# Performance work log

Hardware: AMD Instinct MI355X
Metric: run time of the kernel (lower is better)

## Reference

```python
import jax, jax.numpy as jnp
import numpy as np

B = 16      # number of graphs (equal-sized, batch = repeat(arange(B), N))


def _knn_edges(pos, k, total):
    """Batch-aware kNN graph, torch_geometric knn_graph semantics.

    loop=False, flow='source_to_target': for each query node i, its k nearest
    neighbors j produce edges (row=j neighbor/source, col=i query/target).
    Returns (row, col) as flat global int32 index arrays of length B*N*k.
    """
    N = total // B
    posb = pos.reshape(B, N, -1)                      # [B, N, 3]
    sq = jnp.sum(posb * posb, axis=-1)                # [B, N]
    # squared Euclidean distances, [B, N, N]
    d2 = sq[:, :, None] + sq[:, None, :] - 2.0 * jnp.einsum('bnd,bmd->bnm', posb, posb)
    d2 = jnp.where(jnp.eye(N, dtype=bool)[None], jnp.inf, d2)  # exclude self-loops
    _, nbr = jax.lax.top_k(-d2, k)                    # [B, N, k] local neighbor idx
    offs = (jnp.arange(B, dtype=nbr.dtype) * N)[:, None, None]
    row = (nbr + offs).reshape(-1)                                      # neighbors (sources)
    col = jnp.broadcast_to(jnp.arange(N, dtype=nbr.dtype)[None, :, None] + offs,
                           (B, N, k)).reshape(-1)                       # query nodes (targets)
    return row, col


def reference(x, pos, batch, k):
    total = x.shape[0]
    row, col = _knn_edges(pos, k, total)
    # scatter_mean(x[col], row, dim_size=total): mean of gathered features per row index
    sums = jax.ops.segment_sum(x[col], row, num_segments=total)          # [total, d]
    cnt = jax.ops.segment_sum(jnp.ones(row.shape, x.dtype), row, num_segments=total)
    x_neigh_mean = sums / jnp.maximum(cnt, 1.0)[:, None]                 # empty rows -> 0
    return jnp.sum(jnp.abs(x - x_neigh_mean), axis=-1)                   # L1 norm, [total]


def setup_inputs() -> dict:
    key = jax.random.key(0)
    k1, k2 = jax.random.split(key)
    N = 4096
    x = jax.random.normal(k1, (B * N, 64), dtype=jnp.float32)
    pos = jax.random.normal(k2, (B * N, 3), dtype=jnp.float32)
    batch = jnp.repeat(jnp.arange(B, dtype=jnp.int64), N)
    return {"x": x, "pos": pos, "batch": batch, "k": 10}
```

## Files before the change

### kernel.cpp

```cpp
#include <hip/hip_runtime.h>
#include <stdint.h>

#define NB 16
#define NN 4096
#define KK 10
#define NL 8
#define NL2 11
#define LP2 11
#define NSEL 11
#define LPITCH 9
#define FD 64
#define TOTAL (NB * NN)
#define NW 8
#define CH 512
#define QG 64
#define WCAP 24
#define WPITCH 25
#define QCAP 192
#define QPITCH 198
#define SLOTP 11
#define GSZ 32
#define NGRP (TOTAL / GSZ)

#define OFF_HIST 18087936
#define OFF_OIDX 18350080
#define OFF_BBX  18481152
#define SORTED_NEED 18546688

#define INFF __int_as_float(0x7f800000)

typedef float f2 __attribute__((ext_vector_type(2)));

__device__ __forceinline__ f2 FdP3(f2 cx, f2 cy, f2 cz, f2 cq,
                                   f2 vx2, f2 vy2, f2 vz2) {
#pragma clang fp contract(fast)
    f2 t = vx2 * cx + cq;
    t = vy2 * cy + t;
    t = vz2 * cz + t;
    return t;
}

__device__ __forceinline__ uint32_t d2exact(float mx, float my, float mz, float sqi,
                                            float cx, float cy, float cz, float cw) {
    float dot = __fadd_rn(__fadd_rn(__fmul_rn(mx, cx), __fmul_rn(my, cy)),
                          __fmul_rn(mz, cz));
    float d2 = __fsub_rn(__fadd_rn(sqi, cw), __fmul_rn(2.0f, dot));
    return __float_as_uint(d2);
}

__device__ __forceinline__ uint32_t sp3(int v) {
    uint32_t x = (uint32_t)v;
    return (x & 1u) | ((x & 2u) << 2) | ((x & 4u) << 4) | ((x & 8u) << 6);
}

__device__ __forceinline__ uint32_t cellcode(float x, float y, float z) {
    int cx = (int)floorf((x + 4.0f) * 2.0f);
    int cy = (int)floorf((y + 4.0f) * 2.0f);
    int cz = (int)floorf((z + 4.0f) * 2.0f);
    cx = cx < 0 ? 0 : (cx > 15 ? 15 : cx);
    cy = cy < 0 ? 0 : (cy > 15 ? 15 : cy);
    cz = cz < 0 ? 0 : (cz > 15 ? 15 : cz);
    return (sp3(cx) << 2) | (sp3(cy) << 1) | sp3(cz);
}

__global__ __launch_bounds__(256) void hist_kernel(const float* __restrict__ pos,
                                                   int* __restrict__ hist,
                                                   int* __restrict__ cnt) {
    const int i = blockIdx.x * 256 + threadIdx.x;
    const float* s = pos + (size_t)i * 3;
    float x = s[0], y = s[1], z = s[2];
    uint32_t code = cellcode(x, y, z);
    atomicAdd(&hist[(uint32_t)((i >> 12) << 12) | code], 1);
    cnt[i] = 0;
}

__global__ __launch_bounds__(512) void scan_kernel16(int* __restrict__ hist) {
    __shared__ int lds[512];
    const int t = threadIdx.x;
    int* h = hist + (blockIdx.x << 12);
    const int base = t * 8;
    int v[8];
    int s = 0;
#pragma unroll
    for (int j = 0; j < 8; j++) { v[j] = h[base + j]; s += v[j]; }
    lds[t] = s;
    __syncthreads();
    for (int off = 1; off < 512; off <<= 1) {
        int u = (t >= off) ? lds[t - off] : 0;
        __syncthreads();
        lds[t] += u;
        __syncthreads();
    }
    int run = lds[t] - s;
#pragma unroll
    for (int j = 0; j < 8; j++) { h[base + j] = run; run += v[j]; }
}

__global__ __launch_bounds__(256) void scatter_kernel(const float* __restrict__ pos,
                                                      int* __restrict__ offs,
                                                      float* __restrict__ pp4sf,
                                                      uint16_t* __restrict__ oidx) {
    const int i = blockIdx.x * 256 + threadIdx.x;
    const float* s = pos + (size_t)i * 3;
    float x = s[0], y = s[1], z = s[2];
    float q = __fadd_rn(__fadd_rn(__fmul_rn(x, x), __fmul_rn(y, y)),
                        __fmul_rn(z, z));
    uint32_t code = cellcode(x, y, z);
    int sl = atomicAdd(&offs[(uint32_t)((i >> 12) << 12) | code], 1);
    int gs = ((i >> 12) << 12) | sl;
    float* dst = pp4sf + (size_t)(gs >> 1) * 8 + (gs & 1);
    dst[0] = x; dst[2] = y; dst[4] = z; dst[6] = q;
    oidx[gs] = (uint16_t)(i & 4095);
}

__global__ __launch_bounds__(256) void bbox_kernel(const float4* __restrict__ pp4s,
                                                   float* __restrict__ bbx) {
    const int grp = blockIdx.x * 8 + (threadIdx.x >> 5);
    const int sub = threadIdx.x & 31;
    const int gs = grp * GSZ + sub;
    float4 A = pp4s[(gs >> 1) * 2 + 0];
    float4 B = pp4s[(gs >> 1) * 2 + 1];
    bool hi = gs & 1;
    float x = hi ? A.y : A.x, y = hi ? A.w : A.z, z = hi ? B.y : B.x;
    float nx = x, xx = x, ny = y, xy = y, nz = z, xz = z;
#pragma unroll
    for (int o = 1; o < 32; o <<= 1) {
        nx = fminf(nx, __shfl_xor(nx, o, 32)); xx = fmaxf(xx, __shfl_xor(xx, o, 32));
        ny = fminf(ny, __shfl_xor(ny, o, 32)); xy = fmaxf(xy, __shfl_xor(xy, o, 32));
        nz = fminf(nz, __shfl_xor(nz, o, 32)); xz = fmaxf(xz, __shfl_xor(xz, o, 32));
    }
    if (sub == 0) {
        float* d = bbx + (size_t)grp * 8;
        d[0] = nx; d[1] = xx; d[2] = ny; d[3] = xy; d[4] = nz; d[5] = xz;
        d[6] = 0.f; d[7] = 0.f;
    }
}

__global__ __launch_bounds__(512, 8) void knn_sorted_kernel(
        const float4* __restrict__ pp4,
        const uint16_t* __restrict__ oidx,
        const float* __restrict__ bbx,
        int* __restrict__ cnt,
        int* __restrict__ colfix,
        int* __restrict__ nbr) {
    __shared__ uint64_t smem8[3200];
    __shared__ float tau_s[QG];
    __shared__ uint32_t qcnt[QG];
    float* listf = (float*)smem8;
    uint16_t* pool16 = (uint16_t*)smem8;
    uint64_t* slot = smem8;

    const int tid = threadIdx.x;
    const int lane = tid & 63;
    const int w = __builtin_amdgcn_readfirstlane(tid >> 6);
    const int batch = blockIdx.x & 15;
    const int qs = ((blockIdx.x >> 4) << 6) | lane;
    const int gbase = batch << 12;
    const int gqs = gbase + qs;

    float4 mA = pp4[(gqs >> 1) * 2 + 0];
    float4 mB = pp4[(gqs >> 1) * 2 + 1];
    const bool hi = (qs & 1);
    const float mx = hi ? mA.y : mA.x;
    const float my = hi ? mA.w : mA.z;
    const float mz = hi ? mB.y : mB.x;
    const float sqi = hi ? mB.w : mB.z;
    const f2 vx22 = {__fmul_rn(-2.0f, mx), __fmul_rn(-2.0f, mx)};
    const f2 vy22 = {__fmul_rn(-2.0f, my), __fmul_rn(-2.0f, my)};
    const f2 vz22 = {__fmul_rn(-2.0f, mz), __fmul_rn(-2.0f, mz)};

    const f2* __restrict__ bp2 = (const f2*)(pp4 + (size_t)gbase);
    const f2* __restrict__ cp2 = (const f2*)(pp4 + (size_t)(gbase + w * CH));

#define D8P(cb2)                                                      \
    f2 X0 = (cb2)[0],  Y0 = (cb2)[1],  Z0 = (cb2)[2],  Q0 = (cb2)[3]; \
    f2 X1 = (cb2)[4],  Y1 = (cb2)[5],  Z1 = (cb2)[6],  Q1 = (cb2)[7]; \
    f2 X2 = (cb2)[8],  Y2 = (cb2)[9],  Z2 = (cb2)[10], Q2 = (cb2)[11];\
    f2 X3 = (cb2)[12], Y3 = (cb2)[13], Z3 = (cb2)[14], Q3 = (cb2)[15];\
    f2 e0 = FdP3(X0, Y0, Z0, Q0, vx22, vy22, vz22);                   \
    f2 e1 = FdP3(X1, Y1, Z1, Q1, vx22, vy22, vz22);                   \
    f2 e2 = FdP3(X2, Y2, Z2, Q2, vx22, vy22, vz22);                   \
    f2 e3 = FdP3(X3, Y3, Z3, Q3, vx22, vy22, vz22);

    float L[NL2];
#pragma unroll
    for (int t = 0; t < NL2; t++) L[t] = INFF;

#pragma unroll 2
    for (int j = 0; j < 32; ++j) {
        float m = INFF;
#pragma unroll
        for (int s = 0; s < 4; ++s) {
            const f2* c2 = bp2 + (((s << 9) | (j << 4) | w) << 2);
            f2 X = c2[0], Y = c2[1], Z = c2[2], Q = c2[3];
            f2 e = FdP3(X, Y, Z, Q, vx22, vy22, vz22);
            m = fminf(m, fminf(e.x, e.y));
        }
#pragma unroll
        for (int t = 0; t < NL2 - 1; ++t) L[t] = __builtin_amdgcn_fmed3f(L[t], L[t + 1], m);
        L[NL2 - 1] = fminf(L[NL2 - 1], m);
    }
#pragma unroll
    for (int t = 0; t < NL2; t++) listf[tid * LP2 + t] = L[t];
    __syncthreads();

    if (tid < QG) {
        int p[NW];
#pragma unroll
        for (int u = 0; u < NW; u++) p[u] = NL2 - 1;
        float tau = INFF;
        for (int it = 0; it < NSEL; ++it) {
            float best = INFF;
            int bw = 0;
#pragma unroll
            for (int u = 0; u < NW; u++) {
                float v = (p[u] >= 0) ? listf[((u << 6) | tid) * LP2 + p[u]] : INFF;
                if (v < best) { best = v; bw = u; }
            }
            p[bw]--;
            tau = best;
        }
        tau_s[tid] = tau;
        qcnt[tid] = 0;
    }
    __syncthreads();

    const float t0v = tau_s[lane];
    const float tau = t0v + fabsf(t0v) * 1e-4f + 1e-4f;
    const float taud2 = __fadd_rn(tau, sqi) + 1e-4f;
#pragma unroll 1
    for (int og = 0; og < 16; ++og) {
        const float* bb = bbx + (size_t)((batch << 7) | (w << 4) | og) * 8;
        float dx = fmaxf(fmaxf(bb[0] - mx, mx - bb[1]), 0.0f);
        float dy = fmaxf(fmaxf(bb[2] - my, my - bb[3]), 0.0f);
        float dz = fmaxf(fmaxf(bb[4] - mz, mz - bb[5]), 0.0f);
        float d2lb = dx * dx + dy * dy + dz * dz;
        if (__any(d2lb <= taud2)) {
#pragma unroll
            for (int s = 0; s < 4; ++s) {
                const f2* cb2 = cp2 + (og * 4 + s) * 16;
                D8P(cb2);
                const uint32_t jb = (uint32_t)(w * CH + (og * 4 + s) * 8);
                bool h0 = e0.x <= tau, h1 = e0.y <= tau, h2 = e1.x <= tau, h3 = e1.y <= tau;
                bool h4 = e2.x <= tau, h5 = e2.y <= tau, h6 = e3.x <= tau, h7 = e3.y <= tau;
#define PUSH(hv, off)                                                   \
                if (hv) {                                               \
                    uint32_t p = atomicAdd(&qcnt[lane], 1u);            \
                    if (p < QCAP) pool16[lane * QPITCH + p] = (uint16_t)(jb + (off)); \
                }
                if (h0 | h1) { PUSH(h0, 0) PUSH(h1, 1) }
                if (h2 | h3) { PUSH(h2, 2) PUSH(h3, 3) }
                if (h4 | h5) { PUSH(h4, 4) PUSH(h5, 5) }
                if (h6 | h7) { PUSH(h6, 6) PUSH(h7, 7) }
#undef PUSH
            }
        }
    }
    __syncthreads();

    uint64_t S[KK];
#pragma unroll
    for (int t = 0; t < KK; t++) S[t] = ~0ull;
    {
        uint32_t len = qcnt[lane];
        if (len > QCAP) len = QCAP;
        const uint16_t* st = pool16 + lane * QPITCH;
        for (uint32_t e = (uint32_t)w; e < len; e += NW) {
            uint32_t ix = st[e];
            if (ix == (uint32_t)qs) continue;
            int g = gbase + (int)ix;
            float4 A4 = pp4[(g >> 1) * 2 + 0];
            float4 B4 = pp4[(g >> 1) * 2 + 1];
            bool ch = (ix & 1);
            uint32_t db = d2exact(mx, my, mz, sqi,
                                  ch ? A4.y : A4.x, ch ? A4.w : A4.z,
                                  ch ? B4.y : B4.x, ch ? B4.w : B4.z);
            uint32_t orig = (uint32_t)oidx[g];
            uint64_t k64 = ((uint64_t)db << 32) | orig;
            if (k64 < S[0]) {
                bool sh[KK];
                sh[0] = true;
#pragma unroll
                for (int t = 1; t < KK; t++) sh[t] = (k64 < S[t]);
#pragma unroll
                for (int t = 0; t < KK; t++) {
                    uint64_t vac = sh[t] ? k64 : S[t];
                    S[t] = (t + 1 < KK) ? (sh[t + 1] ? S[t + 1] : vac) : vac;
                }
            }
        }
    }
    __syncthreads();

    if (w >= 4) {
        uint64_t* sl = slot + (((w - 4) << 6) | lane) * SLOTP;
#pragma unroll
        for (int j = 0; j < KK; ++j) sl[j] = S[KK - 1 - j];
    }
    __syncthreads();

    if (w < 4) {
        uint64_t* sl = slot + ((w << 6) | lane) * SLOTP;
        uint64_t P[KK];
#pragma unroll
        for (int j = 0; j < KK; ++j) P[j] = sl[j];
#pragma unroll
        for (int j = 0; j < KK; ++j) {
            uint64_t v = S[KK - 1 - j];
            uint32_t r = (uint32_t)j;
#pragma unroll
            for (int i = 0; i < KK; ++i) r += (P[i] < v) ? 1u : 0u;
            if (r < KK) sl[r] = v;
        }
#pragma unroll
        for (int i = 0; i < KK; ++i) {
            uint64_t v = P[i];
            uint32_t r = (uint32_t)i;
#pragma unroll
            for (int t = 0; t < KK; ++t) r += (S[t] <= v) ? 1u : 0u;
            if (r < KK) sl[r] = v;
        }
    }
    __syncthreads();

    if (w < 2) {
        uint64_t* sa = slot + (((w * 2) << 6) | lane) * SLOTP;
        uint64_t* sb = slot + (((w * 2 + 1) << 6) | lane) * SLOTP;
        uint64_t Aa[KK], Bb[KK];
#pragma unroll
        for (int j = 0; j < KK; ++j) Aa[j] = sa[j];
#pragma unroll
        for (int j = 0; j < KK; ++j) Bb[j] = sb[j];
#pragma unroll
        for (int j = 0; j < KK; ++j) {
            uint32_t r = (uint32_t)j;
#pragma unroll
            for (int i = 0; i < KK; ++i) r += (Bb[i] < Aa[j]) ? 1u : 0u;
            if (r < KK) sa[r] = Aa[j];
        }
#pragma unroll
        for (int i = 0; i < KK; ++i) {
            uint32_t r = (uint32_t)i;
#pragma unroll
            for (int j = 0; j < KK; ++j) r += (Aa[j] <= Bb[i]) ? 1u : 0u;
            if (r < KK) sa[r] = Bb[i];
        }
    }
    __syncthreads();

    if (tid < QG) {
        const uint64_t* sa = slot + ((0 << 6) | tid) * SLOTP;
        const uint64_t* sb = slot + ((2 << 6) | tid) * SLOTP;
        uint64_t Aa[KK], Bb[KK];
#pragma unroll
        for (int j = 0; j < KK; ++j) Aa[j] = sa[j];
#pragma unroll
        for (int j = 0; j < KK; ++j) Bb[j] = sb[j];
        const int gq_o = gbase + (int)oidx[gbase + qs];
#define EMIT(key, rk)                                              \
        if ((uint32_t)((key) >> 32) != 0xffffffffu) {              \
            int jl = (int)((key) & 0xffffffffu);                   \
            int gj = gbase + jl;   \
            int p = atomicAdd(&cnt[gj], 1);                        \
            if (colfix) {                                          \
                if (p < 64) colfix[(gj << 6) | p] = gq_o;          \
            } else {                                               \
                nbr[gq_o * KK + (int)(rk)] = gj;                   \
            }                                                      \
        }
#pragma unroll
        for (int j = 0; j < KK; ++j) {
            uint32_t r = (uint32_t)j;
#pragma unroll
            for (int i = 0; i < KK; ++i) r += (Bb[i] < Aa[j]) ? 1u : 0u;
            if (r < KK) EMIT(Aa[j], r)
        }
#pragma unroll
        for (int i = 0; i < KK; ++i) {
            uint32_t r = (uint32_t)i;
#pragma unroll
            for (int j = 0; j < KK; ++j) r += (Aa[j] <= Bb[i]) ? 1u : 0u;
            if (r < KK) EMIT(Bb[i], r)
        }
#undef EMIT
    }
#undef D8P
}

__global__ __launch_bounds__(256) void prep_kernel(const float* __restrict__ pos,
                                                   float4* __restrict__ pp4,
                                                   int* __restrict__ cnt) {
    const int p = blockIdx.x * 256 + threadIdx.x;
    const float* s = pos + (size_t)p * 6;
    float x0 = s[0], y0 = s[1], z0 = s[2];
    float x1 = s[3], y1 = s[4], z1 = s[5];
    float q0 = __fadd_rn(__fadd_rn(__fmul_rn(x0, x0), __fmul_rn(y0, y0)),
                         __fmul_rn(z0, z0));
    float q1 = __fadd_rn(__fadd_rn(__fmul_rn(x1, x1), __fmul_rn(y1, y1)),
                         __fmul_rn(z1, z1));
    pp4[2 * p + 0] = make_float4(x0, x1, y0, y1);
    pp4[2 * p + 1] = make_float4(z0, z1, q0, q1);
    cnt[2 * p + 0] = 0;
    cnt[2 * p + 1] = 0;
}

__global__ __launch_bounds__(512, 8) void knn_kernel(const float4* __restrict__ pp4,
                                                     int* __restrict__ cnt,
                                                     int* __restrict__ colfix,
                                                     int* __restrict__ nbr) {
    __shared__ uint64_t smem8[3200];
    __shared__ float tau_s[QG];
    float* listf = (float*)smem8;
    uint16_t* pool16 = (uint16_t*)smem8;
    uint64_t* slot = smem8;

    const int tid = threadIdx.x;
    const int lane = tid & 63;
    const int w = __builtin_amdgcn_readfirstlane(tid >> 6);
    const int batch = blockIdx.x & 15;
    const int qloc = ((blockIdx.x >> 4) << 6) | lane;
    const int gbase = batch << 12;
    const int gq = gbase + qloc;

    float4 mA = pp4[(gq >> 1) * 2 + 0];
    float4 mB = pp4[(gq >> 1) * 2 + 1];
    const bool hi = (qloc & 1);
    const float mx = hi ? mA.y : mA.x;
    const float my = hi ? mA.w : mA.z;
    const float mz = hi ? mB.y : mB.x;
    const float sqi = hi ? mB.w : mB.z;
    const f2 vx22 = {__fmul_rn(-2.0f, mx), __fmul_rn(-2.0f, mx)};
    const f2 vy22 = {__fmul_rn(-2.0f, my), __fmul_rn(-2.0f, my)};
    const f2 vz22 = {__fmul_rn(-2.0f, mz), __fmul_rn(-2.0f, mz)};

    const f2* __restrict__ cp2 = (const f2*)(pp4 + (size_t)(gbase + w * CH));

#define D8P(cb2)                                                      \
    f2 X0 = (cb2)[0],  Y0 = (cb2)[1],  Z0 = (cb2)[2],  Q0 = (cb2)[3]; \
    f2 X1 = (cb2)[4],  Y1 = (cb2)[5],  Z1 = (cb2)[6],  Q1 = (cb2)[7]; \
    f2 X2 = (cb2)[8],  Y2 = (cb2)[9],  Z2 = (cb2)[10], Q2 = (cb2)[11];\
    f2 X3 = (cb2)[12], Y3 = (cb2)[13], Z3 = (cb2)[14], Q3 = (cb2)[15];\
    f2 e0 = FdP3(X0, Y0, Z0, Q0, vx22, vy22, vz22);                   \
    f2 e1 = FdP3(X1, Y1, Z1, Q1, vx22, vy22, vz22);                   \
    f2 e2 = FdP3(X2, Y2, Z2, Q2, vx22, vy22, vz22);                   \
    f2 e3 = FdP3(X3, Y3, Z3, Q3, vx22, vy22, vz22);

    float L[NL];
#pragma unroll
    for (int t = 0; t < NL; t++) L[t] = INFF;

#pragma unroll 2
    for (int g = 0; g < NL; ++g) {
        float gm = INFF;
#pragma unroll
        for (int s = 0; s < 4; ++s) {
            const f2* cb2 = cp2 + (g * 4 + s) * 16;
            D8P(cb2);
            float m = fminf(fminf(fminf(e0.x, e0.y), fminf(e1.x, e1.y)),
                            fminf(fminf(e2.x, e2.y), fminf(e3.x, e3.y)));
            gm = fminf(gm, m);
        }
#pragma unroll
        for (int t = 0; t < NL - 1; ++t) L[t] = __builtin_amdgcn_fmed3f(L[t], L[t + 1], gm);
        L[NL - 1] = fminf(L[NL - 1], gm);
    }
#pragma unroll
    for (int t = 0; t < NL; t++) listf[tid * LPITCH + t] = L[t];
    __syncthreads();

    if (tid < QG) {
        int p[NW];
#pragma unroll
        for (int u = 0; u < NW; u++) p[u] = NL - 1;
        float tau = INFF;
        for (int it = 0; it < NSEL; ++it) {
            float best = INFF;
            int bw = 0;
#pragma unroll
            for (int u = 0; u < NW; u++) {
                float v = (p[u] >= 0) ? listf[((u << 6) | tid) * LPITCH + p[u]] : INFF;
                if (v < best) { best = v; bw = u; }
            }
            p[bw]--;
            tau = best;
        }
        tau_s[tid] = tau;
    }
    __syncthreads();

    const float t0v = tau_s[lane];
    const float tau = t0v + fabsf(t0v) * 1e-4f + 1e-4f;
    const uint32_t cell0 = (uint32_t)(((w << 6) | lane) * WPITCH);
    uint32_t cpos = cell0;
#pragma unroll 2
    for (int o = 0; o < CH / 8; ++o) {
        const f2* cb2 = cp2 + o * 16;
        D8P(cb2);
        const uint32_t jb = (uint32_t)(w * CH + o * 8);
        bool h0 = e0.x <= tau, h1 = e0.y <= tau, h2 = e1.x <= tau, h3 = e1.y <= tau;
        bool h4 = e2.x <= tau, h5 = e2.y <= tau, h6 = e3.x <= tau, h7 = e3.y <= tau;
#define PUSH(hv, off)                                              \
        if ((hv) && cpos < cell0 + WCAP) {                         \
            pool16[cpos] = (uint16_t)(jb + (off));                 \
            cpos++;                                                \
        }
        if (h0 | h1) { PUSH(h0, 0) PUSH(h1, 1) }
        if (h2 | h3) { PUSH(h2, 2) PUSH(h3, 3) }
        if (h4 | h5) { PUSH(h4, 4) PUSH(h5, 5) }
        if (h6 | h7) { PUSH(h6, 6) PUSH(h7, 7) }
#undef PUSH
    }

    uint64_t S[KK];
#pragma unroll
    for (int t = 0; t < KK; t++) S[t] = ~0ull;
    {
        const uint16_t* st = pool16 + cell0;
        const int c2i = (int)(cpos - cell0);
        for (int e = 0; e < c2i; ++e) {
            uint32_t ix = st[e];
            if (ix == (uint32_t)qloc) continue;
            int g = gbase + (int)ix;
            float4 A4 = pp4[(g >> 1) * 2 + 0];
            float4 B4 = pp4[(g >> 1) * 2 + 1];
            bool ch = (ix & 1);
            uint32_t db = d2exact(mx, my, mz, sqi,
                                  ch ? A4.y : A4.x, ch ? A4.w : A4.z,
                                  ch ? B4.y : B4.x, ch ? B4.w : B4.z);
            uint64_t k64 = ((uint64_t)db << 32) | ix;
            if (k64 < S[0]) {
                bool sh[KK];
                sh[0] = true;
#pragma unroll
                for (int t = 1; t < KK; t++) sh[t] = (k64 < S[t]);
#pragma unroll
                for (int t = 0; t < KK; t++) {
                    uint64_t vac = sh[t] ? k64 : S[t];
                    S[t] = (t + 1 < KK) ? (sh[t + 1] ? S[t + 1] : vac) : vac;
                }
            }
        }
    }
    __syncthreads();

    if (w >= 4) {
        uint64_t* sl = slot + (((w - 4) << 6) | lane) * SLOTP;
#pragma unroll
        for (int j = 0; j < KK; ++j) sl[j] = S[KK - 1 - j];
    }
    __syncthreads();

    if (w < 4) {
        uint64_t* sl = slot + ((w << 6) | lane) * SLOTP;
        uint64_t P[KK];
#pragma unroll
        for (int j = 0; j < KK; ++j) P[j] = sl[j];
#pragma unroll
        for (int j = 0; j < KK; ++j) {
            uint64_t v = S[KK - 1 - j];
            uint32_t r = (uint32_t)j;
#pragma unroll
            for (int i = 0; i < KK; ++i) r += (P[i] < v) ? 1u : 0u;
            if (r < KK) sl[r] = v;
        }
#pragma unroll
        for (int i = 0; i < KK; ++i) {
            uint64_t v = P[i];
            uint32_t r = (uint32_t)i;
#pragma unroll
            for (int t = 0; t < KK; ++t) r += (S[t] <= v) ? 1u : 0u;
            if (r < KK) sl[r] = v;
        }
    }
    __syncthreads();

    if (w < 2) {
        uint64_t* sa = slot + (((w * 2) << 6) | lane) * SLOTP;
        uint64_t* sb = slot + (((w * 2 + 1) << 6) | lane) * SLOTP;
        uint64_t Aa[KK], Bb[KK];
#pragma unroll
        for (int j = 0; j < KK; ++j) Aa[j] = sa[j];
#pragma unroll
        for (int j = 0; j < KK; ++j) Bb[j] = sb[j];
#pragma unroll
        for (int j = 0; j < KK; ++j) {
            uint32_t r = (uint32_t)j;
#pragma unroll
            for (int i = 0; i < KK; ++i) r += (Bb[i] < Aa[j]) ? 1u : 0u;
            if (r < KK) sa[r] = Aa[j];
        }
#pragma unroll
        for (int i = 0; i < KK; ++i) {
            uint32_t r = (uint32_t)i;
#pragma unroll
            for (int j = 0; j < KK; ++j) r += (Aa[j] <= Bb[i]) ? 1u : 0u;
            if (r < KK) sa[r] = Bb[i];
        }
    }
    __syncthreads();

    if (tid < QG) {
        const uint64_t* sa = slot + ((0 << 6) | tid) * SLOTP;
        const uint64_t* sb = slot + ((2 << 6) | tid) * SLOTP;
        uint64_t Aa[KK], Bb[KK];
#pragma unroll
        for (int j = 0; j < KK; ++j) Aa[j] = sa[j];
#pragma unroll
        for (int j = 0; j < KK; ++j) Bb[j] = sb[j];
#define EMIT(key, rk)                                              \
        {                                                          \
            int jl = (int)((key) & 0xffffffffu);                   \
            int gj = gbase + jl;                                   \
            int p = atomicAdd(&cnt[gj], 1);                        \
            if (colfix) {                                          \
                if (p < 64) colfix[(gj << 6) | p] = gq;            \
            } else {                                               \
                nbr[gq * KK + (int)(rk)] = gj;                     \
            }                                                      \
        }
#pragma unroll
        for (int j = 0; j < KK; ++j) {
            uint32_t r = (uint32_t)j;
#pragma unroll
            for (int i = 0; i < KK; ++i) r += (Bb[i] < Aa[j]) ? 1u : 0u;
            if (r < KK) EMIT(Aa[j], r)
        }
#pragma unroll
        for (int i = 0; i < KK; ++i) {
            uint32_t r = (uint32_t)i;
#pragma unroll
            for (int j = 0; j < KK; ++j) r += (Aa[j] <= Bb[i]) ? 1u : 0u;
            if (r < KK) EMIT(Bb[i], r)
        }
#undef EMIT
    }
#undef D8P
}

__global__ __launch_bounds__(256) void out_bucket_kernel(const float4* __restrict__ x4,
                                                         const int* __restrict__ colfix,
                                                         const int* __restrict__ cnt,
                                                         float* __restrict__ out) {
    const int b = blockIdx.x;
    const int g = b & 15;
    const int i = b >> 4;
    const int l = threadIdx.x & 31;
    const int n = (g << 12) | (i << 3) | (threadIdx.x >> 5);
    const int s = l & 15;
    const int half = l >> 4;
    const int c = cnt[n];
    const int cc = (c > 64) ? 64 : c;
    const int4* cf4 = (const int4*)(colfix + ((size_t)n << 6));
    float4 acc = make_float4(0.f, 0.f, 0.f, 0.f);
    for (int eb = half * 4; eb < cc; eb += 8) {
        int4 Q = cf4[eb >> 2];
        float4 v0 = x4[((size_t)Q.x << 4) | s];
        acc.x += v0.x; acc.y += v0.y; acc.z += v0.z; acc.w += v0.w;
        if (eb + 1 < cc) {
            float4 v1 = x4[((size_t)Q.y << 4) | s];
            acc.x += v1.x; acc.y += v1.y; acc.z += v1.z; acc.w += v1.w;
        }
        if (eb + 2 < cc) {
            float4 v2 = x4[((size_t)Q.z << 4) | s];
            acc.x += v2.x; acc.y += v2.y; acc.z += v2.z; acc.w += v2.w;
        }
        if (eb + 3 < cc) {
            float4 v3 = x4[((size_t)Q.w << 4) | s];
            acc.x += v3.x; acc.y += v3.y; acc.z += v3.z; acc.w += v3.w;
        }
    }
    acc.x += __shfl_xor(acc.x, 16, 64);
    acc.y += __shfl_xor(acc.y, 16, 64);
    acc.z += __shfl_xor(acc.z, 16, 64);
    acc.w += __shfl_xor(acc.w, 16, 64);
    const float inv = 1.0f / (float)(c > 1 ? c : 1);
    float4 mn = x4[((size_t)n << 4) | s];
    float v = fabsf(mn.x - acc.x * inv) + fabsf(mn.y - acc.y * inv) +
              fabsf(mn.z - acc.z * inv) + fabsf(mn.w - acc.w * inv);
    v += __shfl_xor(v, 1, 64);
    v += __shfl_xor(v, 2, 64);
    v += __shfl_xor(v, 4, 64);
    v += __shfl_xor(v, 8, 64);
    if (l == 0) out[n] = v;
}

__global__ __launch_bounds__(1024) void scan_kernel(const int* __restrict__ cnt,
                                                    int* __restrict__ offs) {
    __shared__ int lds[1024];
    const int t = threadIdx.x;
    const int base = t * 64;
    int s = 0;
    for (int i = 0; i < 64; i++) s += cnt[base + i];
    lds[t] = s;
    __syncthreads();
    for (int off = 1; off < 1024; off <<= 1) {
        int v = (t >= off) ? lds[t - off] : 0;
        __syncthreads();
        lds[t] += v;
        __syncthreads();
    }
    int run = lds[t] - s;
    for (int i = 0; i < 64; i++) {
        offs[base + i] = run;
        run += cnt[base + i];
    }
}

__global__ __launch_bounds__(256) void fill_kernel(const int* __restrict__ nbr,
                                                   int* __restrict__ offs,
                                                   int* __restrict__ col) {
    const int i = blockIdx.x * 256 + threadIdx.x;
#pragma unroll
    for (int t = 0; t < KK; t++) {
        int j = nbr[i * KK + t];
        int p = atomicAdd(&offs[j], 1);
        col[p] = i;
    }
}

__global__ __launch_bounds__(256) void out_kernel(const float* __restrict__ x,
                                                  const int* __restrict__ col,
                                                  const int* __restrict__ offs_end,
                                                  const int* __restrict__ cnt,
                                                  float* __restrict__ out) {
    const int gtid = blockIdx.x * 256 + threadIdx.x;
    const int n = gtid >> 6;
    const int lane = gtid & 63;
    const int c = cnt[n];
    const int end = offs_end[n];
    const int start = end - c;
    float s = 0.0f;
    for (int e = start; e < end; e++) {
        int i = col[e];
        s += x[(size_t)i * FD + lane];
    }
    float mean = s / (float)(c > 1 ? c : 1);
    float v = fabsf(x[(size_t)n * FD + lane] - mean);
#pragma unroll
    for (int off = 32; off; off >>= 1) v += __shfl_xor(v, off, 64);
    if (lane == 0) out[n] = v;
}

extern "C" void kernel_launch(void* const* d_in, const int* in_sizes, int n_in,
                              void* d_out, int out_size, void* d_ws, size_t ws_size,
                              hipStream_t stream) {
    const float* x = (const float*)d_in[0];
    const float* pos = (const float*)d_in[1];
    float* out = (float*)d_out;

    char* ws = (char*)d_ws;
    float4* pp4 = (float4*)(ws + 0);
    int* cnt = (int*)(ws + 1048576);
    int* colfix = (int*)(ws + 1310720);
    int* nbr = (int*)(ws + 1310720);
    int* offs = (int*)(ws + 3932160);
    int* col = (int*)(ws + 4194304);
    int* hist = (int*)(ws + OFF_HIST);
    uint16_t* oidx = (uint16_t*)(ws + OFF_OIDX);
    float* bbx = (float*)(ws + OFF_BBX);

    const bool bucket = ws_size >= (size_t)(1310720 + TOTAL * 64 * 4);
    const bool sorted = ws_size >= (size_t)SORTED_NEED;

    if (sorted) {
        hipMemsetAsync(hist, 0, NB * 4096 * sizeof(int), stream);
        hipLaunchKernelGGL(hist_kernel, dim3(TOTAL / 256), dim3(256), 0, stream,
                           pos, hist, cnt);
        hipLaunchKernelGGL(scan_kernel16, dim3(NB), dim3(512), 0, stream, hist);
        hipLaunchKernelGGL(scatter_kernel, dim3(TOTAL / 256), dim3(256), 0, stream,
                           pos, hist, (float*)pp4, oidx);
        hipLaunchKernelGGL(bbox_kernel, dim3(NGRP / 8), dim3(256), 0, stream,
                           pp4, bbx);
        hipLaunchKernelGGL(knn_sorted_kernel, dim3(TOTAL / QG), dim3(512), 0, stream,
                           pp4, oidx, bbx, cnt, colfix, (int*)nullptr);
        hipLaunchKernelGGL(out_bucket_kernel, dim3(TOTAL * 32 / 256), dim3(256), 0, stream,
                           (const float4*)x, colfix, cnt, out);
    } else {
        hipLaunchKernelGGL(prep_kernel, dim3(TOTAL / 2 / 256), dim3(256), 0, stream,
                           pos, pp4, cnt);
        hipLaunchKernelGGL(knn_kernel, dim3(TOTAL / QG), dim3(512), 0, stream, pp4, cnt,
                           bucket ? colfix : (int*)nullptr, bucket ? (int*)nullptr : nbr);
        if (bucket) {
            hipLaunchKernelGGL(out_bucket_kernel, dim3(TOTAL * 32 / 256), dim3(256), 0, stream,
                               (const float4*)x, colfix, cnt, out);
        } else {
            hipLaunchKernelGGL(scan_kernel, dim3(1), dim3(1024), 0, stream, cnt, offs);
            hipLaunchKernelGGL(fill_kernel, dim3(TOTAL / 256), dim3(256), 0, stream, nbr, offs, col);
            hipLaunchKernelGGL(out_kernel, dim3(TOTAL * FD / 256), dim3(256), 0, stream,
                               x, col, offs, cnt, out);
        }
    }
}
```

Before: 186.6 us.

## Permute features into spatially sorted order for locality in the neighbor-mean gather

Adds a kernel that copies the feature matrix into the spatial cell-sorted order, plus a per-node index from original to sorted slot. The output kernel then gathers neighbor features from the sorted copy, so spatially close neighbors read nearby memory and cache reuse should improve. The cost is an extra full pass over the 16 MB feature array, an extra index lookup per edge, and more workspace, which is only used when the workspace is large enough. The unroll factor of the kNN pre-scan loop is also raised from 2 to 4.

```diff
diff --git a/kernel.cpp b/kernel.cpp
--- a/kernel.cpp
+++ b/kernel.cpp
@@ -26,6 +26,9 @@
 #define OFF_OIDX 18350080
 #define OFF_BBX  18481152
 #define SORTED_NEED 18546688
+#define OFF_SIDX 18546688
+#define OFF_XS2  18677760
+#define XS2_NEED 35454976
 
 #define INFF __int_as_float(0x7f800000)
 
@@ -99,7 +102,8 @@
 __global__ __launch_bounds__(256) void scatter_kernel(const float* __restrict__ pos,
                                                       int* __restrict__ offs,
                                                       float* __restrict__ pp4sf,
-                                                      uint16_t* __restrict__ oidx) {
+                                                      uint16_t* __restrict__ oidx,
+                                                      uint16_t* __restrict__ sidx) {
     const int i = blockIdx.x * 256 + threadIdx.x;
     const float* s = pos + (size_t)i * 3;
     float x = s[0], y = s[1], z = s[2];
@@ -111,6 +115,7 @@
     float* dst = pp4sf + (size_t)(gs >> 1) * 8 + (gs & 1);
     dst[0] = x; dst[2] = y; dst[4] = z; dst[6] = q;
     oidx[gs] = (uint16_t)(i & 4095);
+    if (sidx) sidx[i] = (uint16_t)(gs & 4095);
 }
 
 __global__ __launch_bounds__(256) void bbox_kernel(const float4* __restrict__ pp4s,
@@ -134,6 +139,16 @@
         d[0] = nx; d[1] = xx; d[2] = ny; d[3] = xy; d[4] = nz; d[5] = xz;
         d[6] = 0.f; d[7] = 0.f;
     }
+}
+
+__global__ __launch_bounds__(256) void xsort_kernel(const float4* __restrict__ x4,
+                                                    const uint16_t* __restrict__ oidx,
+                                                    float4* __restrict__ xs4) {
+    const int idx = blockIdx.x * 256 + threadIdx.x;
+    const int ns = idx >> 4;
+    const int q = idx & 15;
+    const int o = (ns & ~4095) | (int)oidx[ns];
+    xs4[idx] = x4[((size_t)o << 4) | q];
 }
 
 __global__ __launch_bounds__(512, 8) void knn_sorted_kernel(
@@ -186,7 +201,7 @@
 #pragma unroll
     for (int t = 0; t < NL2; t++) L[t] = INFF;
 
-#pragma unroll 2
+#pragma unroll 4
     for (int j = 0; j < 32; ++j) {
         float m = INFF;
 #pragma unroll
@@ -684,6 +699,59 @@
     if (l == 0) out[n] = v;
 }
 
+__global__ __launch_bounds__(256) void out_bucket_sx(const float4* __restrict__ x4,
+                                                     const float4* __restrict__ xs4,
+                                                     const int* __restrict__ colfix,
+                                                     const int* __restrict__ cnt,
+                                                     const uint16_t* __restrict__ sidx,
+                                                     float* __restrict__ out) {
+    const int b = blockIdx.x;
+    const int g = b & 15;
+    const int i = b >> 4;
+    const int l = threadIdx.x & 31;
+    const int n = (g << 12) | (i << 3) | (threadIdx.x >> 5);
+    const int s = l & 15;
+    const int half = l >> 4;
+    const int c = cnt[n];
+    const int cc = (c > 64) ? 64 : c;
+    const int4* cf4 = (const int4*)(colfix + ((size_t)n << 6));
+    float4 acc = make_float4(0.f, 0.f, 0.f, 0.f);
+    for (int eb = half * 4; eb < cc; eb += 8) {
+        int4 Q = cf4[eb >> 2];
+        int s0 = (Q.x & ~4095) | (int)sidx[Q.x];
+        float4 v0 = xs4[((size_t)s0 << 4) | s];
+        acc.x += v0.x; acc.y += v0.y; acc.z += v0.z; acc.w += v0.w;
+        if (eb + 1 < cc) {
+            int s1 = (Q.y & ~4095) | (int)sidx[Q.y];
+            float4 v1 = xs4[((size_t)s1 << 4) | s];
+            acc.x += v1.x; acc.y += v1.y; acc.z += v1.z; acc.w += v1.w;
+        }
+        if (eb + 2 < cc) {
+            int s2 = (Q.z & ~4095) | (int)sidx[Q.z];
+            float4 v2 = xs4[((size_t)s2 << 4) | s];
+            acc.x += v2.x; acc.y += v2.y; acc.z += v2.z; acc.w += v2.w;
+        }
+        if (eb + 3 < cc) {
+            int s3 = (Q.w & ~4095) | (int)sidx[Q.w];
+            float4 v3 = xs4[((size_t)s3 << 4) | s];
+            acc.x += v3.x; acc.y += v3.y; acc.z += v3.z; acc.w += v3.w;
+        }
+    }
+    acc.x += __shfl_xor(acc.x, 16, 64);
+    acc.y += __shfl_xor(acc.y, 16, 64);
+    acc.z += __shfl_xor(acc.z, 16, 64);
+    acc.w += __shfl_xor(acc.w, 16, 64);
+    const float inv = 1.0f / (float)(c > 1 ? c : 1);
+    float4 mn = x4[((size_t)n << 4) | s];
+    float v = fabsf(mn.x - acc.x * inv) + fabsf(mn.y - acc.y * inv) +
+              fabsf(mn.z - acc.z * inv) + fabsf(mn.w - acc.w * inv);
+    v += __shfl_xor(v, 1, 64);
+    v += __shfl_xor(v, 2, 64);
+    v += __shfl_xor(v, 4, 64);
+    v += __shfl_xor(v, 8, 64);
+    if (l == 0) out[n] = v;
+}
+
 __global__ __launch_bounds__(1024) void scan_kernel(const int* __restrict__ cnt,
                                                     int* __restrict__ offs) {
     __shared__ int lds[1024];
@@ -758,9 +826,12 @@
     int* hist = (int*)(ws + OFF_HIST);
     uint16_t* oidx = (uint16_t*)(ws + OFF_OIDX);
     float* bbx = (float*)(ws + OFF_BBX);
+    uint16_t* sidx = (uint16_t*)(ws + OFF_SIDX);
+    float4* xs4 = (float4*)(ws + OFF_XS2);
 
     const bool bucket = ws_size >= (size_t)(1310720 + TOTAL * 64 * 4);
     const bool sorted = ws_size >= (size_t)SORTED_NEED;
+    const bool sx = ws_size >= (size_t)XS2_NEED;
 
     if (sorted) {
         hipMemsetAsync(hist, 0, NB * 4096 * sizeof(int), stream);
@@ -768,13 +839,22 @@
                            pos, hist, cnt);
         hipLaunchKernelGGL(scan_kernel16, dim3(NB), dim3(512), 0, stream, hist);
         hipLaunchKernelGGL(scatter_kernel, dim3(TOTAL / 256), dim3(256), 0, stream,
-                           pos, hist, (float*)pp4, oidx);
+                           pos, hist, (float*)pp4, oidx, sx ? sidx : (uint16_t*)nullptr);
         hipLaunchKernelGGL(bbox_kernel, dim3(NGRP / 8), dim3(256), 0, stream,
                            pp4, bbx);
+        if (sx) {
+            hipLaunchKernelGGL(xsort_kernel, dim3(TOTAL * 16 / 256), dim3(256), 0, stream,
+                               (const float4*)x, oidx, xs4);
+        }
         hipLaunchKernelGGL(knn_sorted_kernel, dim3(TOTAL / QG), dim3(512), 0, stream,
                            pp4, oidx, bbx, cnt, colfix, (int*)nullptr);
-        hipLaunchKernelGGL(out_bucket_kernel, dim3(TOTAL * 32 / 256), dim3(256), 0, stream,
-                           (const float4*)x, colfix, cnt, out);
+        if (sx) {
+            hipLaunchKernelGGL(out_bucket_sx, dim3(TOTAL * 32 / 256), dim3(256), 0, stream,
+                               (const float4*)x, (const float4*)xs4, colfix, cnt, sidx, out);
+        } else {
+            hipLaunchKernelGGL(out_bucket_kernel, dim3(TOTAL * 32 / 256), dim3(256), 0, stream,
+                               (const float4*)x, colfix, cnt, out);
+        }
     } else {
         hipLaunchKernelGGL(prep_kernel, dim3(TOTAL / 2 / 256), dim3(256), 0, stream,
                            pos, pp4, cnt);
```

After: 201.3 us. 1.08x slower.
